# Performance work log

Measured on AMD Instinct MI355X. Metric: run time of the kernel, lower is better.

## Reference

```python
import jax, jax.numpy as jnp
import numpy as np

H = 1024
NH = 16
DH = H // NH
EPS = 1e-12


def _heads(x):
    # [B,T,H] -> [B,NH,T,DH]
    B, T, _ = x.shape
    return x.reshape(B, T, NH, DH).transpose(0, 2, 1, 3)


def _layernorm(x, g, b):
    mu = jnp.mean(x, axis=-1, keepdims=True)
    var = jnp.mean(jnp.square(x - mu), axis=-1, keepdims=True)
    return (x - mu) * jax.lax.rsqrt(var + EPS) * g + b


def setup_inputs() -> dict:
    key = jax.random.key(0)
    ks = jax.random.split(key, 24)
    B, Tw, Te = 4, 1024, 128
    s = 0.02
    inp = {
        "word_hidden_states": jax.random.normal(ks[0], (B, Tw, H), jnp.float32),
        "entity_hidden_states": jax.random.normal(ks[1], (B, Te, H), jnp.float32),
        "attention_mask": jnp.zeros((B, 1, 1, Tw + Te), jnp.float32),
        "query_pos": jax.random.normal(ks[2], (B, Te, H), jnp.float32),
    }
    names = ["Wq", "Wk", "Wv", "Weq", "Wek", "Wev", "Wo", "Weo"]
    for i, n in enumerate(names):
        inp[n] = jax.random.normal(ks[3 + i], (H, H), jnp.float32) * s
        inp["b" + n[1:]] = jnp.zeros((H,), jnp.float32)
    inp["ln_g"] = jnp.ones((H,), jnp.float32)
    inp["ln_b"] = jnp.zeros((H,), jnp.float32)
    inp["eln_g"] = jnp.ones((H,), jnp.float32)
    inp["eln_b"] = jnp.zeros((H,), jnp.float32)
    return inp


def reference(word_hidden_states, entity_hidden_states, attention_mask, query_pos,
              Wq, bq, Wk, bk, Wv, bv, Weq, beq, Wek, bek, Wev, bev,
              Wo, bo, Weo, beo, ln_g, ln_b, eln_g, eln_b):
    Tw = word_hidden_states.shape[1]
    pos_ent = (entity_hidden_states + query_pos) * 0.5

    # per-stream projections (entity stream has its own e2w projections)
    qw = _heads(word_hidden_states @ Wq + bq)      # [B,NH,Tw,DH]
    qe = _heads(pos_ent @ Weq + beq)               # [B,NH,Te,DH]
    kw = _heads(word_hidden_states @ Wk + bk)
    ke = _heads(pos_ent @ Wek + bek)
    vw = _heads(word_hidden_states @ Wv + bv)
    ve = _heads(entity_hidden_states @ Wev + bev)  # value uses raw entity states

    q = jnp.concatenate([qw, qe], axis=2)          # [B,NH,T,DH]
    k = jnp.concatenate([kw, ke], axis=2)
    v = jnp.concatenate([vw, ve], axis=2)

    scores = jnp.einsum("bhqd,bhkd->bhqk", q, k) / np.sqrt(DH).astype(np.float32)
    scores = scores + attention_mask
    probs = jax.nn.softmax(scores, axis=-1)
    ctx = jnp.einsum("bhqk,bhkd->bhqd", probs, v)  # [B,NH,T,DH]
    B, _, T, _ = ctx.shape
    ctx = ctx.transpose(0, 2, 1, 3).reshape(B, T, H)

    word_self = ctx[:, :Tw, :]
    ent_self = ctx[:, Tw:, :]

    word_out = _layernorm(word_self @ Wo + bo + word_hidden_states, ln_g, ln_b)
    ent_out = _layernorm(ent_self @ Weo + beo + entity_hidden_states, eln_g, eln_b)
    return (word_out, ent_out)
```

## Files before the change

kernel.cpp:

```cpp
#include <hip/hip_runtime.h>
#include <math.h>

#define H_DIM 1024
#define NHEAD 16
#define DHEAD 64
#define T_W 1024
#define T_E 128
#define T_T 1152
#define BATCH 4

typedef __attribute__((ext_vector_type(8))) short s8b;
typedef __attribute__((ext_vector_type(4))) short s4b;
typedef __attribute__((ext_vector_type(4))) float f32x4;

#define LOG2E 1.44269504088896f

__device__ __forceinline__ unsigned short f2bf(float f) {
    unsigned int u = __float_as_uint(f);
    u = (u + 0x7fffu + ((u >> 16) & 1u)) >> 16;
    return (unsigned short)u;
}

__device__ __forceinline__ unsigned int pk_bf16(float a, float b) {
#if __has_builtin(__builtin_amdgcn_cvt_pk_bf16_f32)
    typedef __bf16 bf2 __attribute__((ext_vector_type(2)));
    bf2 r = __builtin_amdgcn_cvt_pk_bf16_f32(a, b);
    return __builtin_bit_cast(unsigned int, r);
#else
    return (unsigned int)f2bf(a) | ((unsigned int)f2bf(b) << 16);
#endif
}

__device__ __forceinline__ float exp2f_fast(float x) {
#if __has_builtin(__builtin_amdgcn_exp2f)
    return __builtin_amdgcn_exp2f(x);
#else
    return exp2f(x);
#endif
}

__device__ __forceinline__ void gld_lds16(const void* g, void* l) {
    __builtin_amdgcn_global_load_lds(
        (const __attribute__((address_space(1))) unsigned int*)g,
        (__attribute__((address_space(3))) unsigned int*)l, 16, 0, 0);
}

struct WPtrs { const float* w[8]; };
__global__ __launch_bounds__(256) void k_prep2(
    const float* __restrict__ word, const float* __restrict__ ent,
    const float* __restrict__ qp, const float* __restrict__ mask,
    unsigned short* __restrict__ word_bf, unsigned short* __restrict__ pe_bf,
    unsigned short* __restrict__ ent_bf, float* __restrict__ mask2,
    WPtrs ws, unsigned short* __restrict__ Wt)
{
    const int bid = blockIdx.x;
    if (bid < 4096) {
        int i = bid * 256 + threadIdx.x;
        float4 v = ((const float4*)word)[i];
        *(uint2*)(word_bf + (size_t)i * 4) =
            make_uint2(pk_bf16(v.x, v.y), pk_bf16(v.z, v.w));
    } else if (bid < 4608) {
        int i = (bid - 4096) * 256 + threadIdx.x;
        float4 a = ((const float4*)ent)[i];
        float4 b = ((const float4*)qp)[i];
        *(uint2*)(ent_bf + (size_t)i * 4) =
            make_uint2(pk_bf16(a.x, a.y), pk_bf16(a.z, a.w));
        *(uint2*)(pe_bf + (size_t)i * 4) =
            make_uint2(pk_bf16((a.x + b.x) * 0.5f, (a.y + b.y) * 0.5f),
                       pk_bf16((a.z + b.z) * 0.5f, (a.w + b.w) * 0.5f));
    } else if (bid < 4626) {
        int i = (bid - 4608) * 256 + threadIdx.x;
        if (i < BATCH * T_T) mask2[i] = mask[i] * LOG2E;
    } else {
        __shared__ float tile[32][33];
        const int id = bid - 4626;
        const int z = id >> 10, rem = id & 1023;
        const int kb = (rem >> 5) * 32, nb = (rem & 31) * 32;
        const float* src = ws.w[z];
        unsigned short* dst = Wt + (size_t)z * H_DIM * H_DIM;
        const int tx = threadIdx.x & 31, ty = threadIdx.x >> 5;
        #pragma unroll
        for (int i = 0; i < 4; i++)
            tile[ty * 4 + i][tx] = src[(size_t)(kb + ty * 4 + i) * H_DIM + nb + tx];
        __syncthreads();
        #pragma unroll
        for (int i = 0; i < 4; i++)
            dst[(size_t)(nb + ty * 4 + i) * H_DIM + kb + tx] =
                f2bf(tile[tx][ty * 4 + i]);
    }
}

struct B6 { const float* b[6]; };
struct O3p { void* o[3]; };

__global__ __launch_bounds__(256) void k_proj(
    const unsigned short* __restrict__ word_bf,
    const unsigned short* __restrict__ pe_bf,
    const unsigned short* __restrict__ ent_bf,
    const unsigned short* __restrict__ Wtbase, B6 biases, O3p outs)
{
    const int z = blockIdx.z;
    const bool isw = blockIdx.y < 32;
    const int Tseq = isw ? T_W : T_E;
    const int toff = isw ? 0 : T_W;
    const int m0 = (isw ? blockIdx.y : (blockIdx.y - 32)) * 128;
    const unsigned short* A = isw ? word_bf : (z == 2 ? ent_bf : pe_bf);
    const int wi = (isw ? 0 : 3) + z;
    const unsigned short* B = Wtbase + (size_t)wi * H_DIM * H_DIM;
    const float* bias = biases.b[wi];
    void* outp = outs.o[z];

    __shared__ unsigned short sm[8192];
    const int t = threadIdx.x;
    const int w = t >> 6, lane = t & 63;
    const int col = lane & 15, quad = lane >> 4;
    const int n0 = blockIdx.x * 128;
    const int wm = w & 1, wn = w >> 1;
    const int rA = t >> 2, kA = (t & 3) * 8;

    f32x4 acc[4][4] = {};

    const unsigned short* gA0 = A + (size_t)(m0 + rA) * H_DIM + kA;
    const unsigned short* gA1 = A + (size_t)(m0 + 64 + rA) * H_DIM + kA;
    const unsigned short* gB0 = B + (size_t)(n0 + rA) * H_DIM + kA;
    const unsigned short* gB1 = B + (size_t)(n0 + 64 + rA) * H_DIM + kA;
    unsigned short* lA0 = &sm[t * 8];
    unsigned short* lA1 = &sm[2048 + t * 8];
    unsigned short* lB0 = &sm[4096 + t * 8];
    unsigned short* lB1 = &sm[6144 + t * 8];

    for (int k0 = 0; k0 < H_DIM; k0 += 32) {
        gld_lds16(gA0 + k0, lA0);
        gld_lds16(gA1 + k0, lA1);
        gld_lds16(gB0 + k0, lB0);
        gld_lds16(gB1 + k0, lB1);
        __syncthreads();
        s8b af[4], bfr[4];
        #pragma unroll
        for (int mt = 0; mt < 4; mt++)
            af[mt] = *(const s8b*)&sm[(wm * 64 + mt * 16 + col) * 32 + quad * 8];
        #pragma unroll
        for (int nt = 0; nt < 4; nt++)
            bfr[nt] = *(const s8b*)&sm[4096 + (wn * 64 + nt * 16 + col) * 32 + quad * 8];
        #pragma unroll
        for (int mt = 0; mt < 4; mt++)
            #pragma unroll
            for (int nt = 0; nt < 4; nt++)
                acc[mt][nt] = __builtin_amdgcn_mfma_f32_16x16x32_bf16(
                    af[mt], bfr[nt], acc[mt][nt], 0, 0, 0);
        __syncthreads();
    }

    #pragma unroll
    for (int mt = 0; mt < 4; mt++) {
        const int mg = m0 + wm * 64 + mt * 16 + quad * 4;
        const int b = mg / Tseq, tt = toff + (mg % Tseq);
        #pragma unroll
        for (int nt = 0; nt < 4; nt++) {
            const int ng = n0 + wn * 64 + nt * 16 + col;
            f32x4 c = acc[mt][nt];
            const float bn = bias[ng];
            if (z < 2) {
                unsigned short* out = (unsigned short*)outp;
                #pragma unroll
                for (int r = 0; r < 4; r++)
                    out[((size_t)b * T_T + tt + r) * H_DIM + ng] = f2bf(c[r] + bn);
            } else {
                unsigned short* out = (unsigned short*)outp;
                *(uint2*)(out + ((size_t)b * H_DIM + ng) * T_T + tt) =
                    make_uint2(pk_bf16(c[0] + bn, c[1] + bn),
                               pk_bf16(c[2] + bn, c[3] + bn));
            }
        }
    }
}

__global__ __launch_bounds__(256) void k_gemm_out(
    const unsigned short* __restrict__ ctx,
    const unsigned short* __restrict__ Wt_o, const unsigned short* __restrict__ Wt_eo,
    const float* __restrict__ bo, const float* __restrict__ beo,
    const float* __restrict__ word, const float* __restrict__ ent,
    float* __restrict__ out_word, float* __restrict__ out_ent)
{
    const int blk = blockIdx.x;
    const bool is_word = blk < 256;
    const int lb = is_word ? blk : blk - 256;
    const int m0 = (lb >> 3) * 128, n0 = (lb & 7) * 128;
    const unsigned short* B = is_word ? Wt_o : Wt_eo;
    const float* bias = is_word ? bo : beo;
    const float* resid = is_word ? word : ent;
    float* out = is_word ? out_word : out_ent;
    const int Tseq = is_word ? T_W : T_E;
    const int toff = is_word ? 0 : T_W;

    __shared__ unsigned short sm[8192];
    const int t = threadIdx.x;
    const int w = t >> 6, lane = t & 63;
    const int col = lane & 15, quad = lane >> 4;
    const int wm = w & 1, wn = w >> 1;
    const int rA = t >> 2, kA = (t & 3) * 8;

    f32x4 acc[4][4] = {};

    const int r0 = m0 + rA, r1 = m0 + 64 + rA;
    const size_t arow0 = (size_t)(r0 / Tseq) * T_T + toff + (r0 % Tseq);
    const size_t arow1 = (size_t)(r1 / Tseq) * T_T + toff + (r1 % Tseq);
    const unsigned short* gA0 = ctx + arow0 * H_DIM + kA;
    const unsigned short* gA1 = ctx + arow1 * H_DIM + kA;
    const unsigned short* gB0 = B + (size_t)(n0 + rA) * H_DIM + kA;
    const unsigned short* gB1 = B + (size_t)(n0 + 64 + rA) * H_DIM + kA;
    unsigned short* lA0 = &sm[t * 8];
    unsigned short* lA1 = &sm[2048 + t * 8];
    unsigned short* lB0 = &sm[4096 + t * 8];
    unsigned short* lB1 = &sm[6144 + t * 8];

    for (int k0 = 0; k0 < H_DIM; k0 += 32) {
        gld_lds16(gA0 + k0, lA0);
        gld_lds16(gA1 + k0, lA1);
        gld_lds16(gB0 + k0, lB0);
        gld_lds16(gB1 + k0, lB1);
        __syncthreads();
        s8b af[4], bfr[4];
        #pragma unroll
        for (int mt = 0; mt < 4; mt++)
            af[mt] = *(const s8b*)&sm[(wm * 64 + mt * 16 + col) * 32 + quad * 8];
        #pragma unroll
        for (int nt = 0; nt < 4; nt++)
            bfr[nt] = *(const s8b*)&sm[4096 + (wn * 64 + nt * 16 + col) * 32 + quad * 8];
        #pragma unroll
        for (int mt = 0; mt < 4; mt++)
            #pragma unroll
            for (int nt = 0; nt < 4; nt++)
                acc[mt][nt] = __builtin_amdgcn_mfma_f32_16x16x32_bf16(
                    af[mt], bfr[nt], acc[mt][nt], 0, 0, 0);
        __syncthreads();
    }

    #pragma unroll
    for (int mt = 0; mt < 4; mt++) {
        const int mg = m0 + wm * 64 + mt * 16 + quad * 4;
        #pragma unroll
        for (int nt = 0; nt < 4; nt++) {
            const int ng = n0 + wn * 64 + nt * 16 + col;
            f32x4 c = acc[mt][nt];
            const float bn = bias[ng];
            #pragma unroll
            for (int r = 0; r < 4; r++) {
                const size_t idx = (size_t)(mg + r) * H_DIM + ng;
                out[idx] = c[r] + bn + resid[idx];
            }
        }
    }
}

__global__ __launch_bounds__(512) void k_attn(
    const unsigned short* __restrict__ q, const unsigned short* __restrict__ k,
    const unsigned short* __restrict__ vt, const float* __restrict__ mask2,
    unsigned short* __restrict__ ctx)
{
    const int tid = threadIdx.x;
    const int w = tid >> 6, lane = tid & 63;
    const int col = lane & 15, quad = lane >> 4;
    const int bh = blockIdx.x / 9;
    const int q0 = (blockIdx.x % 9) * 128 + w * 16;
    const int b = bh >> 4, h = bh & 15;

    __shared__ unsigned short sK[2][64 * 64];
    __shared__ unsigned short sV[2][64 * 64];
    __shared__ __align__(16) unsigned short sP[8][16 * 64];
    unsigned short* sp = &sP[w][0];

    const unsigned short* qp = q + ((size_t)b * T_T + q0) * H_DIM + h * DHEAD;
    const unsigned short* kp = k + (size_t)b * T_T * H_DIM + h * DHEAD;
    const unsigned short* vp = vt + ((size_t)b * H_DIM + h * DHEAD) * T_T;
    const float* mp = mask2 + (size_t)b * T_T;

    const s8b qf0 = *(const s8b*)(qp + (size_t)col * H_DIM + quad * 8);
    const s8b qf1 = *(const s8b*)(qp + (size_t)col * H_DIM + 32 + quad * 8);

    const int rA = tid >> 3;
    const int cA = (tid & 7) ^ (rA & 7);

    const float SC2 = 0.125f * LOG2E;

    f32x4 O[4] = {};
    float l_part = 0.f;

    #define PREFETCH(J0, BUF)                                                        \
        {                                                                            \
            gld_lds16(kp + (size_t)((J0) + rA) * H_DIM + cA * 8,                     \
                      &sK[BUF][0] + tid * 8);                                        \
            gld_lds16(vp + (size_t)rA * T_T + (J0) + cA * 8,                         \
                      &sV[BUF][0] + tid * 8);                                        \
        }

    PREFETCH(0, 0)
    for (int it = 0; it < 18; it++) {
        const int j0 = it * 64;
        __syncthreads();
        if (it < 17) PREFETCH(j0 + 64, (it + 1) & 1)
        const unsigned short* K0 = &sK[it & 1][0];
        const unsigned short* V0 = &sV[it & 1][0];

        float p[16];
        #pragma unroll
        for (int kt = 0; kt < 4; kt++) {
            const int rk = kt * 16 + col;
            const int csw = quad ^ (rk & 7);
            s8b k0f = *(const s8b*)(K0 + rk * 64 + csw * 8);
            s8b k1f = *(const s8b*)(K0 + rk * 64 + (csw ^ 4) * 8);
            f32x4 z = {0.f, 0.f, 0.f, 0.f};
            z = __builtin_amdgcn_mfma_f32_16x16x32_bf16(k0f, qf0, z, 0, 0, 0);
            z = __builtin_amdgcn_mfma_f32_16x16x32_bf16(k1f, qf1, z, 0, 0, 0);
            float4 mv = *(const float4*)(mp + j0 + kt * 16 + quad * 4);
            float mvv[4] = {mv.x, mv.y, mv.z, mv.w};
            #pragma unroll
            for (int r = 0; r < 4; r++) {
                float pe = exp2f_fast(fmaf(z[r], SC2, mvv[r]));
                p[kt * 4 + r] = pe;
                l_part += pe;
            }
        }

        #pragma unroll
        for (int kt = 0; kt < 4; kt++) {
            const int chunk = 2 * kt + (quad >> 1);
            *(uint2*)(sp + col * 64 + ((chunk ^ (col & 7)) * 8) + (quad & 1) * 4) =
                make_uint2(pk_bf16(p[4 * kt], p[4 * kt + 1]),
                           pk_bf16(p[4 * kt + 2], p[4 * kt + 3]));
        }
        const s8b p0 = *(const s8b*)(sp + col * 64 + ((quad ^ (col & 7)) * 8));
        const s8b p1 = *(const s8b*)(sp + col * 64 + (((4 + quad) ^ (col & 7)) * 8));

        #pragma unroll
        for (int dt = 0; dt < 4; dt++) {
            const int rf = dt * 16 + col;
            const int csw = quad ^ (rf & 7);
            s8b v0 = *(const s8b*)(V0 + rf * 64 + csw * 8);
            s8b v1 = *(const s8b*)(V0 + rf * 64 + (csw ^ 4) * 8);
            O[dt] = __builtin_amdgcn_mfma_f32_16x16x32_bf16(v0, p0, O[dt], 0, 0, 0);
            O[dt] = __builtin_amdgcn_mfma_f32_16x16x32_bf16(v1, p1, O[dt], 0, 0, 0);
        }
    }
    #undef PREFETCH

    float l_c = l_part;
    l_c += __shfl_xor(l_c, 16);
    l_c += __shfl_xor(l_c, 32);
    const float inv = 1.f / l_c;
    unsigned short* ob = ctx + ((size_t)b * T_T + q0 + col) * H_DIM + h * DHEAD;
    #pragma unroll
    for (int dt = 0; dt < 4; dt++) {
        *(uint2*)(ob + dt * 16 + quad * 4) =
            make_uint2(pk_bf16(O[dt][0] * inv, O[dt][1] * inv),
                       pk_bf16(O[dt][2] * inv, O[dt][3] * inv));
    }
}

__global__ __launch_bounds__(256) void k_layernorm(float* __restrict__ x,
                                                   const float* __restrict__ g0,
                                                   const float* __restrict__ b0,
                                                   const float* __restrict__ g1,
                                                   const float* __restrict__ b1)
{
    const int row = blockIdx.x;
    const float* g = row < 4096 ? g0 : g1;
    const float* bta = row < 4096 ? b0 : b1;
    float* p = x + (size_t)row * H_DIM;
    const int t = threadIdx.x;
    float vals[4];
    float s = 0.f, ss = 0.f;
    #pragma unroll
    for (int i = 0; i < 4; i++) {
        float v = p[t + 256 * i];
        vals[i] = v;
        s += v;
        ss += v * v;
    }
    #pragma unroll
    for (int o = 32; o > 0; o >>= 1) {
        s += __shfl_xor(s, o);
        ss += __shfl_xor(ss, o);
    }
    __shared__ float red[2][4];
    const int wid = t >> 6, lane = t & 63;
    if (lane == 0) { red[0][wid] = s; red[1][wid] = ss; }
    __syncthreads();
    s = red[0][0] + red[0][1] + red[0][2] + red[0][3];
    ss = red[1][0] + red[1][1] + red[1][2] + red[1][3];
    float mu = s * (1.0f / H_DIM);
    float var = ss * (1.0f / H_DIM) - mu * mu;
    float r = rsqrtf(var + 1e-12f);
    #pragma unroll
    for (int i = 0; i < 4; i++) {
        int idx = t + 256 * i;
        p[idx] = (vals[i] - mu) * r * g[idx] + bta[idx];
    }
}

extern "C" void kernel_launch(void* const* d_in, const int* in_sizes, int n_in,
                              void* d_out, int out_size, void* d_ws, size_t ws_size,
                              hipStream_t stream) {
    const float* word = (const float*)d_in[0];
    const float* ent  = (const float*)d_in[1];
    const float* mask = (const float*)d_in[2];
    const float* qpos = (const float*)d_in[3];
    const float* Wq  = (const float*)d_in[4];  const float* bq  = (const float*)d_in[5];
    const float* Wk  = (const float*)d_in[6];  const float* bk  = (const float*)d_in[7];
    const float* Wv  = (const float*)d_in[8];  const float* bv  = (const float*)d_in[9];
    const float* Weq = (const float*)d_in[10]; const float* beq = (const float*)d_in[11];
    const float* Wek = (const float*)d_in[12]; const float* bek = (const float*)d_in[13];
    const float* Wev = (const float*)d_in[14]; const float* bev = (const float*)d_in[15];
    const float* Wo  = (const float*)d_in[16]; const float* bo  = (const float*)d_in[17];
    const float* Weo = (const float*)d_in[18]; const float* beo = (const float*)d_in[19];
    const float* ln_g  = (const float*)d_in[20]; const float* ln_b  = (const float*)d_in[21];
    const float* eln_g = (const float*)d_in[22]; const float* eln_b = (const float*)d_in[23];

    char* ws = (char*)d_ws;
    unsigned short* word_bf = (unsigned short*)(ws);
    unsigned short* pe_bf   = (unsigned short*)(ws + 8388608);
    unsigned short* ent_bf  = (unsigned short*)(ws + 9437184);
    float*          mask2   = (float*)(ws + 10466304);
    unsigned short* Wt      = (unsigned short*)(ws + 10485760);
    unsigned short* qb      = (unsigned short*)(ws + 27262976);
    unsigned short* kb      = (unsigned short*)(ws + 36700160);
    unsigned short* vt      = (unsigned short*)(ws + 46137344);
    unsigned short* ctx     = (unsigned short*)(ws + 55574528);

    float* out_word = (float*)d_out;
    float* out_ent  = out_word + 4194304;

    const size_t WSZ = (size_t)H_DIM * H_DIM;
    unsigned short* Wt_o  = Wt + 6 * WSZ;
    unsigned short* Wt_eo = Wt + 7 * WSZ;

    WPtrs wp = {{Wq, Wk, Wv, Weq, Wek, Wev, Wo, Weo}};
    k_prep2<<<dim3(12818), 256, 0, stream>>>(word, ent, qpos, mask,
                                             word_bf, pe_bf, ent_bf, mask2, wp, Wt);

    B6 bb = {{bq, bk, bv, beq, bek, bev}};
    O3p ow = {{qb, kb, vt}};
    k_proj<<<dim3(8, 36, 3), 256, 0, stream>>>(word_bf, pe_bf, ent_bf, Wt, bb, ow);

    k_attn<<<dim3(NHEAD * BATCH * 9), 512, 0, stream>>>(qb, kb, vt, mask2, ctx);

    k_gemm_out<<<dim3(288), 256, 0, stream>>>(ctx, Wt_o, Wt_eo, bo, beo,
                                              word, ent, out_word, out_ent);

    k_layernorm<<<dim3(4608), 256, 0, stream>>>(out_word, ln_g, ln_b, eln_g, eln_b);
}
```

Before: 279.4 us.

## Use 64x128 GEMM tiles with K=64 steps and XOR-swizzled LDS layout

```diff
diff --git a/kernel.cpp b/kernel.cpp
--- a/kernel.cpp
+++ b/kernel.cpp
@@ -93,6 +93,7 @@
 struct B6 { const float* b[6]; };
 struct O3p { void* o[3]; };
 
+
 __global__ __launch_bounds__(256) void k_proj(
     const unsigned short* __restrict__ word_bf,
     const unsigned short* __restrict__ pe_bf,
@@ -100,60 +101,65 @@
     const unsigned short* __restrict__ Wtbase, B6 biases, O3p outs)
 {
     const int z = blockIdx.z;
-    const bool isw = blockIdx.y < 32;
+    const bool isw = blockIdx.y < 64;
     const int Tseq = isw ? T_W : T_E;
     const int toff = isw ? 0 : T_W;
-    const int m0 = (isw ? blockIdx.y : (blockIdx.y - 32)) * 128;
+    const int m0 = (isw ? blockIdx.y : (blockIdx.y - 64)) * 64;
     const unsigned short* A = isw ? word_bf : (z == 2 ? ent_bf : pe_bf);
     const int wi = (isw ? 0 : 3) + z;
     const unsigned short* B = Wtbase + (size_t)wi * H_DIM * H_DIM;
     const float* bias = biases.b[wi];
     void* outp = outs.o[z];
 
-    __shared__ unsigned short sm[8192];
+    __shared__ unsigned short sm[12288];
     const int t = threadIdx.x;
     const int w = t >> 6, lane = t & 63;
     const int col = lane & 15, quad = lane >> 4;
     const int n0 = blockIdx.x * 128;
     const int wm = w & 1, wn = w >> 1;
-    const int rA = t >> 2, kA = (t & 3) * 8;
-
-    f32x4 acc[4][4] = {};
-
-    const unsigned short* gA0 = A + (size_t)(m0 + rA) * H_DIM + kA;
-    const unsigned short* gA1 = A + (size_t)(m0 + 64 + rA) * H_DIM + kA;
-    const unsigned short* gB0 = B + (size_t)(n0 + rA) * H_DIM + kA;
-    const unsigned short* gB1 = B + (size_t)(n0 + 64 + rA) * H_DIM + kA;
-    unsigned short* lA0 = &sm[t * 8];
-    unsigned short* lA1 = &sm[2048 + t * 8];
-    unsigned short* lB0 = &sm[4096 + t * 8];
-    unsigned short* lB1 = &sm[6144 + t * 8];
-
-    for (int k0 = 0; k0 < H_DIM; k0 += 32) {
-        gld_lds16(gA0 + k0, lA0);
-        gld_lds16(gA1 + k0, lA1);
-        gld_lds16(gB0 + k0, lB0);
-        gld_lds16(gB1 + k0, lB1);
-        __syncthreads();
-        s8b af[4], bfr[4];
-        #pragma unroll
-        for (int mt = 0; mt < 4; mt++)
-            af[mt] = *(const s8b*)&sm[(wm * 64 + mt * 16 + col) * 32 + quad * 8];
-        #pragma unroll
-        for (int nt = 0; nt < 4; nt++)
-            bfr[nt] = *(const s8b*)&sm[4096 + (wn * 64 + nt * 16 + col) * 32 + quad * 8];
-        #pragma unroll
-        for (int mt = 0; mt < 4; mt++)
-            #pragma unroll
-            for (int nt = 0; nt < 4; nt++)
-                acc[mt][nt] = __builtin_amdgcn_mfma_f32_16x16x32_bf16(
-                    af[mt], bfr[nt], acc[mt][nt], 0, 0, 0);
-        __syncthreads();
-    }
-
-    #pragma unroll
-    for (int mt = 0; mt < 4; mt++) {
-        const int mg = m0 + wm * 64 + mt * 16 + quad * 4;
+
+    f32x4 acc[2][4] = {};
+
+    const int rs = t >> 3;
+    const int gch = (t & 7) ^ (rs & 7);
+    const unsigned short* gA = A + (size_t)(m0 + rs) * H_DIM + gch * 8;
+    const unsigned short* gB = B + (size_t)(n0 + rs) * H_DIM + gch * 8;
+
+    for (int k0 = 0; k0 < H_DIM; k0 += 64) {
+        gld_lds16(gA + k0, &sm[t * 8]);
+        gld_lds16(gA + (size_t)32 * H_DIM + k0, &sm[2048 + t * 8]);
+        gld_lds16(gB + k0, &sm[4096 + t * 8]);
+        gld_lds16(gB + (size_t)32 * H_DIM + k0, &sm[6144 + t * 8]);
+        gld_lds16(gB + (size_t)64 * H_DIM + k0, &sm[8192 + t * 8]);
+        gld_lds16(gB + (size_t)96 * H_DIM + k0, &sm[10240 + t * 8]);
+        __syncthreads();
+        #pragma unroll
+        for (int kk = 0; kk < 2; kk++) {
+            s8b af[2], bfr[4];
+            #pragma unroll
+            for (int mt = 0; mt < 2; mt++) {
+                const int r = wm * 32 + mt * 16 + col;
+                af[mt] = *(const s8b*)&sm[r * 64 + (((kk * 4 + quad) ^ (r & 7)) * 8)];
+            }
+            #pragma unroll
+            for (int nt = 0; nt < 4; nt++) {
+                const int r = wn * 64 + nt * 16 + col;
+                bfr[nt] = *(const s8b*)&sm[4096 + r * 64 +
+                                           (((kk * 4 + quad) ^ (r & 7)) * 8)];
+            }
+            #pragma unroll
+            for (int mt = 0; mt < 2; mt++)
+                #pragma unroll
+                for (int nt = 0; nt < 4; nt++)
+                    acc[mt][nt] = __builtin_amdgcn_mfma_f32_16x16x32_bf16(
+                        af[mt], bfr[nt], acc[mt][nt], 0, 0, 0);
+        }
+        __syncthreads();
+    }
+
+    #pragma unroll
+    for (int mt = 0; mt < 2; mt++) {
+        const int mg = m0 + wm * 32 + mt * 16 + quad * 4;
         const int b = mg / Tseq, tt = toff + (mg % Tseq);
         #pragma unroll
         for (int nt = 0; nt < 4; nt++) {
@@ -183,9 +189,9 @@
     float* __restrict__ out_word, float* __restrict__ out_ent)
 {
     const int blk = blockIdx.x;
-    const bool is_word = blk < 256;
-    const int lb = is_word ? blk : blk - 256;
-    const int m0 = (lb >> 3) * 128, n0 = (lb & 7) * 128;
+    const bool is_word = blk < 512;
+    const int lb = is_word ? blk : blk - 512;
+    const int m0 = (lb >> 3) * 64, n0 = (lb & 7) * 128;
     const unsigned short* B = is_word ? Wt_o : Wt_eo;
     const float* bias = is_word ? bo : beo;
     const float* resid = is_word ? word : ent;
@@ -193,52 +199,55 @@
     const int Tseq = is_word ? T_W : T_E;
     const int toff = is_word ? 0 : T_W;
 
-    __shared__ unsigned short sm[8192];
+    __shared__ unsigned short sm[12288];
     const int t = threadIdx.x;
     const int w = t >> 6, lane = t & 63;
     const int col = lane & 15, quad = lane >> 4;
     const int wm = w & 1, wn = w >> 1;
-    const int rA = t >> 2, kA = (t & 3) * 8;
-
-    f32x4 acc[4][4] = {};
-
-    const int r0 = m0 + rA, r1 = m0 + 64 + rA;
-    const size_t arow0 = (size_t)(r0 / Tseq) * T_T + toff + (r0 % Tseq);
-    const size_t arow1 = (size_t)(r1 / Tseq) * T_T + toff + (r1 % Tseq);
-    const unsigned short* gA0 = ctx + arow0 * H_DIM + kA;
-    const unsigned short* gA1 = ctx + arow1 * H_DIM + kA;
-    const unsigned short* gB0 = B + (size_t)(n0 + rA) * H_DIM + kA;
-    const unsigned short* gB1 = B + (size_t)(n0 + 64 + rA) * H_DIM + kA;
-    unsigned short* lA0 = &sm[t * 8];
-    unsigned short* lA1 = &sm[2048 + t * 8];
-    unsigned short* lB0 = &sm[4096 + t * 8];
-    unsigned short* lB1 = &sm[6144 + t * 8];
-
-    for (int k0 = 0; k0 < H_DIM; k0 += 32) {
-        gld_lds16(gA0 + k0, lA0);
-        gld_lds16(gA1 + k0, lA1);
-        gld_lds16(gB0 + k0, lB0);
-        gld_lds16(gB1 + k0, lB1);
-        __syncthreads();
-        s8b af[4], bfr[4];
-        #pragma unroll
-        for (int mt = 0; mt < 4; mt++)
-            af[mt] = *(const s8b*)&sm[(wm * 64 + mt * 16 + col) * 32 + quad * 8];
-        #pragma unroll
-        for (int nt = 0; nt < 4; nt++)
-            bfr[nt] = *(const s8b*)&sm[4096 + (wn * 64 + nt * 16 + col) * 32 + quad * 8];
-        #pragma unroll
-        for (int mt = 0; mt < 4; mt++)
-            #pragma unroll
-            for (int nt = 0; nt < 4; nt++)
-                acc[mt][nt] = __builtin_amdgcn_mfma_f32_16x16x32_bf16(
-                    af[mt], bfr[nt], acc[mt][nt], 0, 0, 0);
-        __syncthreads();
-    }
-
-    #pragma unroll
-    for (int mt = 0; mt < 4; mt++) {
-        const int mg = m0 + wm * 64 + mt * 16 + quad * 4;
+
+    f32x4 acc[2][4] = {};
+
+    const int rs = t >> 3;
+    const int gch = (t & 7) ^ (rs & 7);
+    const size_t arow = (size_t)(m0 / Tseq) * T_T + toff + (m0 % Tseq) + rs;
+    const unsigned short* gA = ctx + arow * H_DIM + gch * 8;
+    const unsigned short* gB = B + (size_t)(n0 + rs) * H_DIM + gch * 8;
+
+    for (int k0 = 0; k0 < H_DIM; k0 += 64) {
+        gld_lds16(gA + k0, &sm[t * 8]);
+        gld_lds16(gA + (size_t)32 * H_DIM + k0, &sm[2048 + t * 8]);
+        gld_lds16(gB + k0, &sm[4096 + t * 8]);
+        gld_lds16(gB + (size_t)32 * H_DIM + k0, &sm[6144 + t * 8]);
+        gld_lds16(gB + (size_t)64 * H_DIM + k0, &sm[8192 + t * 8]);
+        gld_lds16(gB + (size_t)96 * H_DIM + k0, &sm[10240 + t * 8]);
+        __syncthreads();
+        #pragma unroll
+        for (int kk = 0; kk < 2; kk++) {
+            s8b af[2], bfr[4];
+            #pragma unroll
+            for (int mt = 0; mt < 2; mt++) {
+                const int r = wm * 32 + mt * 16 + col;
+                af[mt] = *(const s8b*)&sm[r * 64 + (((kk * 4 + quad) ^ (r & 7)) * 8)];
+            }
+            #pragma unroll
+            for (int nt = 0; nt < 4; nt++) {
+                const int r = wn * 64 + nt * 16 + col;
+                bfr[nt] = *(const s8b*)&sm[4096 + r * 64 +
+                                           (((kk * 4 + quad) ^ (r & 7)) * 8)];
+            }
+            #pragma unroll
+            for (int mt = 0; mt < 2; mt++)
+                #pragma unroll
+                for (int nt = 0; nt < 4; nt++)
+                    acc[mt][nt] = __builtin_amdgcn_mfma_f32_16x16x32_bf16(
+                        af[mt], bfr[nt], acc[mt][nt], 0, 0, 0);
+        }
+        __syncthreads();
+    }
+
+    #pragma unroll
+    for (int mt = 0; mt < 2; mt++) {
+        const int mg = m0 + wm * 32 + mt * 16 + quad * 4;
         #pragma unroll
         for (int nt = 0; nt < 4; nt++) {
             const int ng = n0 + wn * 64 + nt * 16 + col;
@@ -440,11 +449,11 @@
 
     B6 bb = {{bq, bk, bv, beq, bek, bev}};
     O3p ow = {{qb, kb, vt}};
-    k_proj<<<dim3(8, 36, 3), 256, 0, stream>>>(word_bf, pe_bf, ent_bf, Wt, bb, ow);
+    k_proj<<<dim3(8, 72, 3), 256, 0, stream>>>(word_bf, pe_bf, ent_bf, Wt, bb, ow);
 
     k_attn<<<dim3(NHEAD * BATCH * 9), 512, 0, stream>>>(qb, kb, vt, mask2, ctx);
 
-    k_gemm_out<<<dim3(288), 256, 0, stream>>>(ctx, Wt_o, Wt_eo, bo, beo,
+    k_gemm_out<<<dim3(576), 256, 0, stream>>>(ctx, Wt_o, Wt_eo, bo, beo,
                                               word, ent, out_word, out_ent);
 
     k_layernorm<<<dim3(4608), 256, 0, stream>>>(out_word, ln_g, ln_b, eln_g, eln_b);
```

New measurement: 260.9 us. -6.6%, faster.
